# Performance work log

Hardware: AMD Instinct MI355X
Metric: run time of the kernel (lower is better)

The kernel has to match this reference:

```python
import jax, jax.numpy as jnp
import numpy as np

MODEL_DIM = 1024
HEADS = 16
HEAD_DIM = MODEL_DIM // HEADS
OUT_DIM = 1024
B, S = 2, 2048


def setup_inputs() -> dict:
    key = jax.random.key(0)
    ks = jax.random.split(key, 10)
    scale = 1.0 / np.sqrt(MODEL_DIM)
    return {
        "query": jax.random.normal(ks[0], (B, S, MODEL_DIM), dtype=jnp.float32),
        "bank": jax.random.normal(ks[1], (B, S, MODEL_DIM), dtype=jnp.float32),
        "Wq": jax.random.normal(ks[2], (MODEL_DIM, MODEL_DIM), dtype=jnp.float32) * scale,
        "bq": jnp.zeros((MODEL_DIM,), dtype=jnp.float32),
        "Wk": jax.random.normal(ks[3], (MODEL_DIM, MODEL_DIM), dtype=jnp.float32) * scale,
        "bk": jnp.zeros((MODEL_DIM,), dtype=jnp.float32),
        "Wv": jax.random.normal(ks[4], (MODEL_DIM, MODEL_DIM), dtype=jnp.float32) * scale,
        "bv": jnp.zeros((MODEL_DIM,), dtype=jnp.float32),
        "Wo": jax.random.normal(ks[5], (OUT_DIM, MODEL_DIM), dtype=jnp.float32) * scale,
        "bo": jnp.zeros((OUT_DIM,), dtype=jnp.float32),
    }


def _split_heads(x):
    # [B, S, D] -> [B, H, S, hd]
    b, s, _ = x.shape
    return x.reshape(b, s, HEADS, HEAD_DIM).transpose(0, 2, 1, 3)


def reference(query, bank, Wq, bq, Wk, bk, Wv, bv, Wo, bo):
    # Linear projections (torch Linear: x @ W.T + b)
    q = _split_heads(query @ Wq.T + bq)  # [B,H,Sq,hd]
    k = _split_heads(bank @ Wk.T + bk)   # [B,H,Sk,hd]
    v = _split_heads(bank @ Wv.T + bv)   # [B,H,Sk,hd]
    score_scale = jnp.sqrt(jnp.float32(HEAD_DIM))
    scores = jnp.einsum("bhqd,bhkd->bhqk", q / score_scale, k)  # [B,H,Sq,Sk]
    attn = jax.nn.softmax(scores, axis=-1)
    # dropout is identity in eval-mode reference
    ctx = jnp.einsum("bhqk,bhkd->bhqd", attn, v)  # [B,H,Sq,hd]
    b, h, sq, hd = ctx.shape
    ctx = ctx.transpose(0, 2, 1, 3).reshape(b, sq, MODEL_DIM)
    return ctx @ Wo.T + bo
```

## Files before the change

### kernel.cpp

```cpp
#include <hip/hip_runtime.h>


#define BDIM   2
#define SDIM   2048
#define DDIM   1024
#define HEADS  16
#define HD     64
#define MROWS  (BDIM * SDIM)

typedef float  f32x4  __attribute__((ext_vector_type(4)));
typedef __bf16 bf16x8 __attribute__((ext_vector_type(8)));
typedef __bf16 bf16x4 __attribute__((ext_vector_type(4)));

#define QSCALE 0.18033688011112042f

__device__ __forceinline__ void stage16(const void* g, void* l) {
    __builtin_amdgcn_global_load_lds((const __attribute__((address_space(1))) void*)g,
                                     (__attribute__((address_space(3))) void*)l,
                                     16, 0, 0);
}

__global__ __launch_bounds__(256) void cvt_all(
    const float* __restrict__ q, const float* __restrict__ bank,
    const float* __restrict__ Wq, const float* __restrict__ Wk,
    const float* __restrict__ Wv, const float* __restrict__ Wo,
    __bf16* __restrict__ xq, __bf16* __restrict__ xkv,
    __bf16* __restrict__ wq, __bf16* __restrict__ wk,
    __bf16* __restrict__ wv, __bf16* __restrict__ wo) {
    const int i = blockIdx.x * 256 + threadIdx.x;
    const float* in;
    __bf16* out;
    int off;
    if (i < 524288)       { in = q;    out = xq;  off = i; }
    else if (i < 1048576) { in = bank; out = xkv; off = i - 524288; }
    else {
        const int j = i - 1048576;
        const int sel = j >> 17;
        off = j & 131071;
        in  = (sel == 0) ? Wq : (sel == 1) ? Wk : (sel == 2) ? Wv : Wo;
        out = (sel == 0) ? wq : (sel == 1) ? wk : (sel == 2) ? wv : wo;
    }
    const float4* p = (const float4*)in;
    float4 a = p[2 * off];
    float4 c = p[2 * off + 1];
    bf16x8 o;
    o[0] = (__bf16)a.x; o[1] = (__bf16)a.y; o[2] = (__bf16)a.z; o[3] = (__bf16)a.w;
    o[4] = (__bf16)c.x; o[5] = (__bf16)c.y; o[6] = (__bf16)c.z; o[7] = (__bf16)c.w;
    *(bf16x8*)(out + 8 * off) = o;
}

template <int MODE>
__global__ __launch_bounds__(256) void gemm_bt(
    const __bf16* __restrict__ Aq, const __bf16* __restrict__ Akv,
    const __bf16* __restrict__ W0, const __bf16* __restrict__ W1,
    const __bf16* __restrict__ W2,
    const float* __restrict__ b0, const float* __restrict__ b1,
    const float* __restrict__ b2,
    __bf16* __restrict__ Qo, __bf16* __restrict__ Ko, __bf16* __restrict__ Vo,
    float* __restrict__ Fo) {
    constexpr int NF = (MODE == 2) ? 2 : 4;
    constexpr int NCOL = NF * 32;
    __shared__ __align__(16) __bf16 ldsA[128 * 32];
    __shared__ __align__(16) __bf16 ldsB[(NCOL)*32];

    const int t = threadIdx.x;
    const int l = t & 63;
    const int w = t >> 6;
    const int z = (MODE == 0) ? (int)blockIdx.z : 0;

    const __bf16* A  = (MODE == 0 && z != 0) ? Akv : Aq;
    const __bf16* Wm = (z == 0) ? W0 : (z == 1 ? W1 : W2);
    const float*  bias = (z == 0) ? b0 : (z == 1 ? b1 : b2);

    const int row0 = blockIdx.y * 128;
    const int col0 = blockIdx.x * NCOL;

    const __bf16* ga = A  + (size_t)(row0 + (t >> 2)) * DDIM + (t & 3) * 8;
    const __bf16* gb = Wm + (size_t)(col0 + (t >> 2)) * DDIM + (t & 3) * 8;
    __bf16* la = ldsA + (t & ~63) * 8;
    __bf16* lb = ldsB + (t & ~63) * 8;

    const int wm = w >> 1, wn = w & 1;
    const int aoff = (wm * 64 + (l & 15)) * 32 + (l >> 4) * 8;
    const int boff = (wn * (NF * 16) + (l & 15)) * 32 + (l >> 4) * 8;

    f32x4 acc[4][NF] = {};

    for (int kb = 0; kb < DDIM; kb += 32) {
        __syncthreads();
        stage16(ga + kb,             la);
        stage16(ga + kb + 64 * DDIM, la + 2048);
        stage16(gb + kb,             lb);
        if constexpr (MODE == 0)
            stage16(gb + kb + 64 * DDIM, lb + 2048);
        __syncthreads();

        bf16x8 af[4], bf[NF];
#pragma unroll
        for (int m = 0; m < 4; ++m) af[m] = *(const bf16x8*)(ldsA + aoff + m * 16 * 32);
#pragma unroll
        for (int n = 0; n < NF; ++n) bf[n] = *(const bf16x8*)(ldsB + boff + n * 16 * 32);
#pragma unroll
        for (int m = 0; m < 4; ++m)
#pragma unroll
            for (int n = 0; n < NF; ++n)
                acc[m][n] = __builtin_amdgcn_mfma_f32_16x16x32_bf16(af[m], bf[n], acc[m][n], 0, 0, 0);
    }

#pragma unroll
    for (int m = 0; m < 4; ++m) {
        const int rbase = row0 + wm * 64 + m * 16 + (l >> 4) * 4;
#pragma unroll
        for (int n = 0; n < NF; ++n) {
            const int col = col0 + wn * (NF * 16) + n * 16 + (l & 15);
            const float bv = bias[col];
            if constexpr (MODE == 0) {
                const int hh = col >> 6, d = col & 63;
#pragma unroll
                for (int j = 0; j < 4; ++j) {
                    const int r = rbase + j;
                    const int b = r >> 11, s = r & 2047;
                    const float v = acc[m][n][j] + bv;
                    if (z == 0) {
                        Qo[(((b * HEADS + hh) * SDIM + s) << 6) + d] = (__bf16)(v * QSCALE);
                    } else if (z == 1) {
                        Ko[(((b * HEADS + hh) * SDIM + s) << 6) + d] = (__bf16)v;
                    } else {
                        Vo[(((b * HEADS + hh) * HD + d) << 11) + s] = (__bf16)v;
                    }
                }
            } else {
#pragma unroll
                for (int j = 0; j < 4; ++j) {
                    Fo[(size_t)(rbase + j) * DDIM + col] = acc[m][n][j] + bv;
                }
            }
        }
    }
}

__global__ __launch_bounds__(512) void attn_fwd(const __bf16* __restrict__ Qb,
                                                const __bf16* __restrict__ Kb,
                                                const __bf16* __restrict__ Vtb,
                                                __bf16* __restrict__ Cb) {
    __shared__ __align__(16) __bf16 ldsK[2][2][64 * 64];
    __shared__ __align__(16) __bf16 ldsV[2][2][64 * 64];

    const int t = threadIdx.x;
    const int l = t & 63;
    const int w = t >> 6;
    const int i15 = l & 15;
    const int q4 = l >> 4;

    const int bid  = blockIdx.x;
    const int xcd  = bid & 7;
    const int wloc = bid >> 3;
    const int bh   = xcd * 4 + (wloc >> 4);
    const int qb   = wloc & 15;
    const int b    = bh >> 4;
    const int h    = bh & 15;
    const size_t base = (size_t)bh * SDIM * HD;
    const int q0 = qb * 128;

    const __bf16* qp = Qb + base + (size_t)(q0 + w * 16 + i15) * HD + q4 * 8;
    const bf16x8 qf0 = *(const bf16x8*)(qp);
    const bf16x8 qf1 = *(const bf16x8*)(qp + 32);

    const int r0 = t >> 3;
    const int sl = (t & 7) ^ (r0 & 7);
    const int sig0 = ((r0 >> 5) << 5) | (((r0 >> 2) & 3) << 3)
                   | (((r0 >> 4) & 1) << 2) | (r0 & 3);
    const __bf16* gk = Kb  + base + (size_t)sig0 * HD + sl * 8;
    const __bf16* gv = Vtb + base + (size_t)r0 * SDIM + sl * 8;
    const int wb = (t & ~63) * 8;

    const int xr = i15 & 7;
    int off[4][2];
#pragma unroll
    for (int n = 0; n < 4; ++n)
#pragma unroll
        for (int hh = 0; hh < 2; ++hh)
            off[n][hh] = (n * 16 + i15) * 64 + (((hh * 4 + q4) ^ xr) << 3);

    bf16x8 ones;
#pragma unroll
    for (int j = 0; j < 8; ++j) ones[j] = (__bf16)1.0f;

    f32x4 c[4] = {};
    f32x4 lsum = {};

    stage16(gk,           &ldsK[0][0][wb]);
    stage16(gk + 64 * HD, &ldsK[0][1][wb]);
    stage16(gv,           &ldsV[0][0][wb]);
    stage16(gv + 64,      &ldsV[0][1][wb]);

#pragma unroll 2
    for (int r = 0; r < SDIM / 128; ++r) {
        const int bb = r & 1;
        __syncthreads();

        if (r + 1 < SDIM / 128) {
            const int s0 = (r + 1) * 128;
            stage16(gk + (size_t)s0 * HD,        &ldsK[bb ^ 1][0][wb]);
            stage16(gk + (size_t)(s0 + 64) * HD, &ldsK[bb ^ 1][1][wb]);
            stage16(gv + s0,                     &ldsV[bb ^ 1][0][wb]);
            stage16(gv + s0 + 64,                &ldsV[bb ^ 1][1][wb]);
        }

        const __bf16* lk0 = &ldsK[bb][0][0];
        const __bf16* lk1 = &ldsK[bb][1][0];
        const __bf16* lv0 = &ldsV[bb][0][0];
        const __bf16* lv1 = &ldsV[bb][1][0];

        f32x4 sA[4] = {}, sB[4] = {};
        __builtin_amdgcn_s_setprio(1);
#pragma unroll
        for (int n = 0; n < 4; ++n) {
            bf16x8 k0 = *(const bf16x8*)(lk0 + off[n][0]);
            bf16x8 k1 = *(const bf16x8*)(lk0 + off[n][1]);
            sA[n] = __builtin_amdgcn_mfma_f32_16x16x32_bf16(k0, qf0, sA[n], 0, 0, 0);
            sA[n] = __builtin_amdgcn_mfma_f32_16x16x32_bf16(k1, qf1, sA[n], 0, 0, 0);
        }
#pragma unroll
        for (int n = 0; n < 4; ++n) {
            bf16x8 k0 = *(const bf16x8*)(lk1 + off[n][0]);
            bf16x8 k1 = *(const bf16x8*)(lk1 + off[n][1]);
            sB[n] = __builtin_amdgcn_mfma_f32_16x16x32_bf16(k0, qf0, sB[n], 0, 0, 0);
            sB[n] = __builtin_amdgcn_mfma_f32_16x16x32_bf16(k1, qf1, sB[n], 0, 0, 0);
        }
        __builtin_amdgcn_s_setprio(0);

#pragma unroll
        for (int n = 0; n < 4; ++n)
#pragma unroll
            for (int j = 0; j < 4; ++j) {
                sA[n][j] = exp2f(sA[n][j]);
                sB[n][j] = exp2f(sB[n][j]);
            }

        bf16x8 paA0, paB0, paA1, paB1;
#pragma unroll
        for (int j = 0; j < 4; ++j) {
            paA0[j]     = (__bf16)sA[0][j];
            paA0[j + 4] = (__bf16)sA[1][j];
            paB0[j]     = (__bf16)sA[2][j];
            paB0[j + 4] = (__bf16)sA[3][j];
            paA1[j]     = (__bf16)sB[0][j];
            paA1[j + 4] = (__bf16)sB[1][j];
            paB1[j]     = (__bf16)sB[2][j];
            paB1[j + 4] = (__bf16)sB[3][j];
        }

        __builtin_amdgcn_s_setprio(1);
        lsum = __builtin_amdgcn_mfma_f32_16x16x32_bf16(ones, paA0, lsum, 0, 0, 0);
        lsum = __builtin_amdgcn_mfma_f32_16x16x32_bf16(ones, paB0, lsum, 0, 0, 0);
        lsum = __builtin_amdgcn_mfma_f32_16x16x32_bf16(ones, paA1, lsum, 0, 0, 0);
        lsum = __builtin_amdgcn_mfma_f32_16x16x32_bf16(ones, paB1, lsum, 0, 0, 0);
#pragma unroll
        for (int n2 = 0; n2 < 4; ++n2) {
            bf16x8 v0 = *(const bf16x8*)(lv0 + off[n2][0]);
            bf16x8 v1 = *(const bf16x8*)(lv0 + off[n2][1]);
            c[n2] = __builtin_amdgcn_mfma_f32_16x16x32_bf16(v0, paA0, c[n2], 0, 0, 0);
            c[n2] = __builtin_amdgcn_mfma_f32_16x16x32_bf16(v1, paB0, c[n2], 0, 0, 0);
            bf16x8 u0 = *(const bf16x8*)(lv1 + off[n2][0]);
            bf16x8 u1 = *(const bf16x8*)(lv1 + off[n2][1]);
            c[n2] = __builtin_amdgcn_mfma_f32_16x16x32_bf16(u0, paA1, c[n2], 0, 0, 0);
            c[n2] = __builtin_amdgcn_mfma_f32_16x16x32_bf16(u1, paB1, c[n2], 0, 0, 0);
        }
        __builtin_amdgcn_s_setprio(0);
    }

    const float inv = 1.0f / lsum[0];
    const int q = q0 + w * 16 + i15;
#pragma unroll
    for (int n2 = 0; n2 < 4; ++n2) {
        bf16x4 o;
#pragma unroll
        for (int j = 0; j < 4; ++j) o[j] = (__bf16)(c[n2][j] * inv);
        *(bf16x4*)(Cb + (size_t)(b * SDIM + q) * DDIM + h * HD + n2 * 16 + q4 * 4) = o;
    }
}

extern "C" void kernel_launch(void* const* d_in, const int* in_sizes, int n_in,
                              void* d_out, int out_size, void* d_ws, size_t ws_size,
                              hipStream_t stream) {
    const float* query = (const float*)d_in[0];
    const float* bank  = (const float*)d_in[1];
    const float* Wq = (const float*)d_in[2];
    const float* bq = (const float*)d_in[3];
    const float* Wk = (const float*)d_in[4];
    const float* bk = (const float*)d_in[5];
    const float* Wv = (const float*)d_in[6];
    const float* bv = (const float*)d_in[7];
    const float* Wo = (const float*)d_in[8];
    const float* bo = (const float*)d_in[9];
    float* out = (float*)d_out;

    char* ws = (char*)d_ws;
    __bf16* xq  = (__bf16*)(ws);
    __bf16* xkv = (__bf16*)(ws + (8u  << 20));
    __bf16* wq  = (__bf16*)(ws + (16u << 20));
    __bf16* wk  = (__bf16*)(ws + (18u << 20));
    __bf16* wv  = (__bf16*)(ws + (20u << 20));
    __bf16* wo  = (__bf16*)(ws + (22u << 20));
    __bf16* qbuf = (__bf16*)(ws + (24u << 20));
    __bf16* kbuf = (__bf16*)(ws + (32u << 20));
    __bf16* vtbuf = (__bf16*)(ws + (40u << 20));
    __bf16* ctx = xq;

    cvt_all<<<6144, 256, 0, stream>>>(query, bank, Wq, Wk, Wv, Wo,
                                      xq, xkv, wq, wk, wv, wo);

    gemm_bt<0><<<dim3(8, 32, 3), 256, 0, stream>>>(
        xq, xkv, wq, wk, wv, bq, bk, bv, qbuf, kbuf, vtbuf, nullptr);

    attn_fwd<<<512, 512, 0, stream>>>(qbuf, kbuf, vtbuf, ctx);

    gemm_bt<2><<<dim3(16, 32, 1), 256, 0, stream>>>(
        ctx, nullptr, wo, nullptr, nullptr, bo, nullptr, nullptr,
        nullptr, nullptr, nullptr, out);
}
```

Baseline: 128.5 us.

## Double GEMM K-tile to 64 with XOR-swizzled LDS layout

```diff
diff --git a/kernel.cpp b/kernel.cpp
--- a/kernel.cpp
+++ b/kernel.cpp
@@ -60,8 +60,8 @@
     float* __restrict__ Fo) {
     constexpr int NF = (MODE == 2) ? 2 : 4;
     constexpr int NCOL = NF * 32;
-    __shared__ __align__(16) __bf16 ldsA[128 * 32];
-    __shared__ __align__(16) __bf16 ldsB[(NCOL)*32];
+    __shared__ __align__(16) __bf16 ldsA[128 * 64];
+    __shared__ __align__(16) __bf16 ldsB[NCOL * 64];
 
     const int t = threadIdx.x;
     const int l = t & 63;
@@ -75,36 +75,59 @@
     const int row0 = blockIdx.y * 128;
     const int col0 = blockIdx.x * NCOL;
 
-    const __bf16* ga = A  + (size_t)(row0 + (t >> 2)) * DDIM + (t & 3) * 8;
-    const __bf16* gb = Wm + (size_t)(col0 + (t >> 2)) * DDIM + (t & 3) * 8;
+    const int srow = t >> 3;
+    const int sg   = (t & 7) ^ (srow & 7);
+    const __bf16* ga = A  + (size_t)(row0 + srow) * DDIM + sg * 8;
+    const __bf16* gb = Wm + (size_t)(col0 + srow) * DDIM + sg * 8;
     __bf16* la = ldsA + (t & ~63) * 8;
     __bf16* lb = ldsB + (t & ~63) * 8;
 
     const int wm = w >> 1, wn = w & 1;
-    const int aoff = (wm * 64 + (l & 15)) * 32 + (l >> 4) * 8;
-    const int boff = (wn * (NF * 16) + (l & 15)) * 32 + (l >> 4) * 8;
+    const int i15 = l & 15;
+    const int q4 = l >> 4;
+    const int xr = i15 & 7;
+
+    int ao[4][2], bo[NF][2];
+#pragma unroll
+    for (int m = 0; m < 4; ++m)
+#pragma unroll
+        for (int h = 0; h < 2; ++h)
+            ao[m][h] = (wm * 64 + m * 16 + i15) * 64 + (((h * 4 + q4) ^ xr) << 3);
+#pragma unroll
+    for (int n = 0; n < NF; ++n)
+#pragma unroll
+        for (int h = 0; h < 2; ++h)
+            bo[n][h] = (wn * (NF * 16) + n * 16 + i15) * 64 + (((h * 4 + q4) ^ xr) << 3);
 
     f32x4 acc[4][NF] = {};
 
-    for (int kb = 0; kb < DDIM; kb += 32) {
+    for (int kb = 0; kb < DDIM; kb += 64) {
         __syncthreads();
         stage16(ga + kb,             la);
-        stage16(ga + kb + 64 * DDIM, la + 2048);
+        stage16(ga + kb + 32 * DDIM, la + 2048);
+        stage16(ga + kb + 64 * DDIM, la + 4096);
+        stage16(ga + kb + 96 * DDIM, la + 6144);
         stage16(gb + kb,             lb);
-        if constexpr (MODE == 0)
-            stage16(gb + kb + 64 * DDIM, lb + 2048);
+        stage16(gb + kb + 32 * DDIM, lb + 2048);
+        if constexpr (MODE == 0) {
+            stage16(gb + kb + 64 * DDIM, lb + 4096);
+            stage16(gb + kb + 96 * DDIM, lb + 6144);
+        }
         __syncthreads();
 
-        bf16x8 af[4], bf[NF];
-#pragma unroll
-        for (int m = 0; m < 4; ++m) af[m] = *(const bf16x8*)(ldsA + aoff + m * 16 * 32);
-#pragma unroll
-        for (int n = 0; n < NF; ++n) bf[n] = *(const bf16x8*)(ldsB + boff + n * 16 * 32);
-#pragma unroll
-        for (int m = 0; m < 4; ++m)
-#pragma unroll
-            for (int n = 0; n < NF; ++n)
-                acc[m][n] = __builtin_amdgcn_mfma_f32_16x16x32_bf16(af[m], bf[n], acc[m][n], 0, 0, 0);
+#pragma unroll
+        for (int h = 0; h < 2; ++h) {
+            bf16x8 af[4], bf[NF];
+#pragma unroll
+            for (int m = 0; m < 4; ++m) af[m] = *(const bf16x8*)(ldsA + ao[m][h]);
+#pragma unroll
+            for (int n = 0; n < NF; ++n) bf[n] = *(const bf16x8*)(ldsB + bo[n][h]);
+#pragma unroll
+            for (int m = 0; m < 4; ++m)
+#pragma unroll
+                for (int n = 0; n < NF; ++n)
+                    acc[m][n] = __builtin_amdgcn_mfma_f32_16x16x32_bf16(af[m], bf[n], acc[m][n], 0, 0, 0);
+        }
     }
 
 #pragma unroll
```

After: 136.7 us. 1.06x slower.
